# Kernel optimization log

Measured on AMD Instinct MI355X. Metric: run time of the kernel, lower is better.

Reference implementation:

```python
import jax, jax.numpy as jnp
import numpy as np

N_NODES = 50000
N_EDGES = 800000
D_IN = 256
D_HID = 256
D_OUT = 16
N_GRAPHS = 128
DROPOUT_P = 0.5


def setup_inputs() -> dict:
    key = jax.random.key(0)
    ks = jax.random.split(key, 8)
    x = jax.random.normal(ks[0], (N_NODES, D_IN), dtype=jnp.float32)
    edge_index = jax.random.randint(ks[1], (2, N_EDGES), 0, N_NODES, dtype=jnp.int64)
    edge_weight = jax.random.uniform(ks[2], (N_EDGES,), dtype=jnp.float32)
    index = jnp.sort(jax.random.randint(ks[3], (N_NODES,), 0, N_GRAPHS, dtype=jnp.int64))
    W1 = jax.random.normal(ks[4], (D_IN, D_HID), dtype=jnp.float32) / np.sqrt(D_IN)
    b1 = jnp.zeros((D_HID,), dtype=jnp.float32)
    fc_W = jax.random.normal(ks[5], (D_HID, D_OUT), dtype=jnp.float32) / np.sqrt(D_HID)
    fc_b = jnp.zeros((D_OUT,), dtype=jnp.float32)
    return {"x": x, "edge_index": edge_index, "edge_weight": edge_weight,
            "index": index, "W1": W1, "b1": b1, "fc_W": fc_W, "fc_b": fc_b}


def gcn_conv(x, edge_index, edge_weight, W, b):
    # PyG GCNConv: add self loops (weight 1), symmetric degree norm, linear-then-propagate.
    n = x.shape[0]
    loops = jnp.arange(n, dtype=edge_index.dtype)
    row = jnp.concatenate([edge_index[0], loops])   # source nodes
    col = jnp.concatenate([edge_index[1], loops])   # target nodes (aggregation)
    ew = jnp.concatenate([edge_weight, jnp.ones((n,), dtype=x.dtype)])
    deg = jax.ops.segment_sum(ew, col, num_segments=n)
    dinv = jnp.where(deg > 0, jax.lax.rsqrt(deg), 0.0)
    norm = dinv[row] * ew * dinv[col]               # [E+N]
    h = x @ W                                       # [N, hid]
    msg = norm[:, None] * h[row]                    # gather + scale
    out = jax.ops.segment_sum(msg, col, num_segments=n)  # scatter-add
    return out + b


def reference(x, edge_index, edge_weight, index, W1, b1, fc_W, fc_b):
    h = gcn_conv(x, edge_index, edge_weight, W1, b1)
    h = jax.nn.relu(h)
    # dropout (training mode, p=0.5) with a fixed key for determinism
    keep = jax.random.bernoulli(jax.random.key(42), 1.0 - DROPOUT_P, h.shape)
    h = jnp.where(keep, h / (1.0 - DROPOUT_P), 0.0)
    # global mean pool over graph ids
    sums = jax.ops.segment_sum(h, index, num_segments=N_GRAPHS)          # [G, hid]
    cnts = jax.ops.segment_sum(jnp.ones((h.shape[0],), h.dtype), index, num_segments=N_GRAPHS)
    pooled = sums / jnp.maximum(cnts, 1.0)[:, None]
    return pooled @ fc_W + fc_b
```

## Files before the change

kernel.cpp:

```cpp
#include <hip/hip_runtime.h>
#include <hip/hip_fp16.h>
#include <stdint.h>

#define N_NODES  50000
#define N_EDGES  800000
#define D        256
#define D_OUT    16
#define N_GRAPHS 128
#define NB_SCAN  196


typedef short bf16x8 __attribute__((ext_vector_type(8)));
typedef float f32x4  __attribute__((ext_vector_type(4)));
typedef float f32x2  __attribute__((ext_vector_type(2)));

__device__ __forceinline__ uint32_t rotl32(uint32_t x, int d) {
    return (x << d) | (x >> (32 - d));
}

__device__ __forceinline__ void threefry2x32(uint32_t k0, uint32_t k1,
                                             uint32_t c0, uint32_t c1,
                                             uint32_t& o0, uint32_t& o1) {
    uint32_t ks2 = k0 ^ k1 ^ 0x1BD11BDAu;
    uint32_t x0 = c0 + k0, x1 = c1 + k1;
    x0 += x1; x1 = rotl32(x1, 13); x1 ^= x0;
    x0 += x1; x1 = rotl32(x1, 15); x1 ^= x0;
    x0 += x1; x1 = rotl32(x1, 26); x1 ^= x0;
    x0 += x1; x1 = rotl32(x1, 6);  x1 ^= x0;
    x0 += k1; x1 += ks2 + 1u;
    x0 += x1; x1 = rotl32(x1, 17); x1 ^= x0;
    x0 += x1; x1 = rotl32(x1, 29); x1 ^= x0;
    x0 += x1; x1 = rotl32(x1, 16); x1 ^= x0;
    x0 += x1; x1 = rotl32(x1, 24); x1 ^= x0;
    x0 += ks2; x1 += k0 + 2u;
    x0 += x1; x1 = rotl32(x1, 13); x1 ^= x0;
    x0 += x1; x1 = rotl32(x1, 15); x1 ^= x0;
    x0 += x1; x1 = rotl32(x1, 26); x1 ^= x0;
    x0 += x1; x1 = rotl32(x1, 6);  x1 ^= x0;
    x0 += k0; x1 += k1 + 3u;
    x0 += x1; x1 = rotl32(x1, 17); x1 ^= x0;
    x0 += x1; x1 = rotl32(x1, 29); x1 ^= x0;
    x0 += x1; x1 = rotl32(x1, 16); x1 ^= x0;
    x0 += x1; x1 = rotl32(x1, 24); x1 ^= x0;
    x0 += k1; x1 += ks2 + 4u;
    x0 += x1; x1 = rotl32(x1, 13); x1 ^= x0;
    x0 += x1; x1 = rotl32(x1, 15); x1 ^= x0;
    x0 += x1; x1 = rotl32(x1, 26); x1 ^= x0;
    x0 += x1; x1 = rotl32(x1, 6);  x1 ^= x0;
    x0 += ks2; x1 += k0 + 5u;
    o0 = x0; o1 = x1;
}

__device__ __forceinline__ bool dropout_keep(uint32_t i) {
    uint32_t o0, o1;
    threefry2x32(0u, 42u, 0u, i, o0, o1);
    return ((o0 ^ o1) & 0x80000000u) == 0u;
}

__device__ __forceinline__ uint32_t bf16_rne(float f) {
    uint32_t u = __float_as_uint(f);
    return (u + 0x7FFFu + ((u >> 16) & 1u)) >> 16;
}

__global__ __launch_bounds__(256) void k_init(const float* __restrict__ W,
                                              ushort* __restrict__ wt,
                                              double* degsum, float* sums,
                                              int2* __restrict__ edge) {
    int t = threadIdx.x;
    if (blockIdx.x < 16) {
        __shared__ float td[64][65];
        int kb = blockIdx.x & 3, nb = blockIdx.x >> 2;
        int nl = t & 63, r4 = t >> 6;
#pragma unroll
        for (int i = 0; i < 16; i++) {
            int kl = r4 + 4 * i;
            td[kl][nl] = W[(size_t)(kb * 64 + kl) * 256 + nb * 64 + nl];
        }
        __syncthreads();
        int kp = t & 31, nl2 = t >> 5;
        uint32_t* wt32 = (uint32_t*)wt;
#pragma unroll
        for (int i = 0; i < 8; i++) {
            int n = nl2 + 8 * i;
            uint32_t p = bf16_rne(td[2 * kp][n]) | (bf16_rne(td[2 * kp + 1][n]) << 16);
            wt32[((size_t)(nb * 64 + n) * 256 + kb * 64 + 2 * kp) >> 1] = p;
        }
    } else {
        int i = (blockIdx.x - 16) * 256 + t;
        if (i < N_NODES) degsum[i] = 0.0;
        if (i < N_GRAPHS * D) sums[i] = 0.0f;
        if (i < 16) edge[N_EDGES + i] = make_int2(0, 0);
    }
}

__global__ __launch_bounds__(256) void k_edeg(const int* __restrict__ ei,
                                              const float* __restrict__ ew,
                                              double* __restrict__ degsum) {
    int e = blockIdx.x * 256 + threadIdx.x;
    int c = ei[N_EDGES + e];
    atomicAdd(&degsum[c], 4294967296.0 + (double)ew[e]);
}

__global__ __launch_bounds__(256) void k_scan1(const double* __restrict__ degsum,
                                               float* __restrict__ dinv,
                                               int* __restrict__ start,
                                               int* __restrict__ partial) {
    __shared__ int sd[256];
    int t = threadIdx.x;
    int i = blockIdx.x * 256 + t;
    int cnt = 0;
    if (i < N_NODES) {
        double val = degsum[i];
        cnt = (int)(val * (1.0 / 4294967296.0));
        float deg = (float)(val - (double)cnt * 4294967296.0) + 1.0f;
        dinv[i] = rsqrtf(deg);
        start[i] = cnt;
    }
    sd[t] = cnt;
    __syncthreads();
    for (int d = 128; d > 0; d >>= 1) {
        if (t < d) sd[t] += sd[t + d];
        __syncthreads();
    }
    if (t == 0) partial[blockIdx.x] = sd[0];
}

__global__ __launch_bounds__(256) void k_scan3(int* __restrict__ start,
                                               const int* __restrict__ partial) {
    __shared__ int sp[256];
    __shared__ int so[256];
    __shared__ int sd[256];
    int t = threadIdx.x;
    int pv = (t < NB_SCAN) ? partial[t] : 0;
    sp[t] = pv; so[t] = pv;
    __syncthreads();
    for (int d = 1; d < 256; d <<= 1) {
        int u = (t >= d) ? sp[t - d] : 0;
        __syncthreads();
        sp[t] += u;
        __syncthreads();
    }
    int base = sp[blockIdx.x] - so[blockIdx.x];

    int i = blockIdx.x * 256 + t;
    int v = (i < N_NODES) ? start[i] : 0;
    sd[t] = v;
    __syncthreads();
    for (int d = 1; d < 256; d <<= 1) {
        int u = (t >= d) ? sd[t - d] : 0;
        __syncthreads();
        sd[t] += u;
        __syncthreads();
    }
    if (i < N_NODES) start[i] = base + sd[t] - v;
}

__global__ __launch_bounds__(256) void k_fill(const int* __restrict__ ei,
                                              const float* __restrict__ ew,
                                              int* __restrict__ start,
                                              int2* __restrict__ edge) {
    int e = blockIdx.x * 256 + threadIdx.x;
    int r = ei[e];
    int c = ei[N_EDGES + e];
    int pos = atomicAdd(&start[c], 1);
    edge[pos] = make_int2(r * 32, __float_as_int(ew[e]));
}

__device__ __forceinline__ int swz(int row, int kByte) {
    return (row << 9) + (kByte ^ ((row & 7) << 4));
}

__global__ __launch_bounds__(256) void k_gemm(const float* __restrict__ x,
                                              const ushort* __restrict__ wt,
                                              const float* __restrict__ dinv,
                                              uint8_t* __restrict__ hb) {
    __shared__ __align__(16) char smem[73728];
    __shared__ float sdinv[64];
    int tid = threadIdx.x;
    int Mbase = blockIdx.x * 64;

    if (tid < 64) {
        int node = Mbase + tid; if (node >= N_NODES) node = N_NODES - 1;
        sdinv[tid] = dinv[node];
    }
    const float4* xv = (const float4*)x;
#pragma unroll
    for (int i = 0; i < 16; i++) {
        int f = tid + i * 256;
        int r = f >> 6;
        int c4 = f & 63;
        int node = Mbase + r; if (node >= N_NODES) node = N_NODES - 1;
        float4 v = xv[(size_t)node * 64 + c4];
        uint32_t p0 = bf16_rne(v.x) | (bf16_rne(v.y) << 16);
        uint32_t p1 = bf16_rne(v.z) | (bf16_rne(v.w) << 16);
        *(uint2*)(smem + swz(r, c4 * 8)) = make_uint2(p0, p1);
    }

    int l = tid & 63;
    int w = tid >> 6;
    int wr = w >> 1, wc = w & 1;
    int lr = l & 15;
    int kg = l >> 4;
    int drow = (l >> 4) * 4;
    int dcol = l & 15;
    const uint4* wt4 = (const uint4*)wt;
    ushort* c_lds = (ushort*)(smem + 65536);

    for (int nb = 0; nb < 4; nb++) {
#pragma unroll
        for (int i = 0; i < 8; i++) {
            int f = tid + i * 256;
            int r = f >> 5;
            int c = f & 31;
            uint4 v = wt4[(size_t)(nb * 64 + r) * 32 + c];
            *(uint4*)(smem + 32768 + swz(r, c * 16)) = v;
        }
        __syncthreads();

        f32x4 acc00 = {0.f, 0.f, 0.f, 0.f};
        f32x4 acc01 = acc00, acc10 = acc00, acc11 = acc00;
#pragma unroll
        for (int ks = 0; ks < 8; ks++) {
            int kB = ks * 64 + kg * 16;
            bf16x8 a0 = *(const bf16x8*)(smem + swz(wr * 32 + lr, kB));
            bf16x8 a1 = *(const bf16x8*)(smem + swz(wr * 32 + 16 + lr, kB));
            bf16x8 b0 = *(const bf16x8*)(smem + 32768 + swz(wc * 32 + lr, kB));
            bf16x8 b1 = *(const bf16x8*)(smem + 32768 + swz(wc * 32 + 16 + lr, kB));
            acc00 = __builtin_amdgcn_mfma_f32_16x16x32_bf16(a0, b0, acc00, 0, 0, 0);
            acc01 = __builtin_amdgcn_mfma_f32_16x16x32_bf16(a0, b1, acc01, 0, 0, 0);
            acc10 = __builtin_amdgcn_mfma_f32_16x16x32_bf16(a1, b0, acc10, 0, 0, 0);
            acc11 = __builtin_amdgcn_mfma_f32_16x16x32_bf16(a1, b1, acc11, 0, 0, 0);
        }
#pragma unroll
        for (int r = 0; r < 4; r++) {
            int lr0 = wr * 32 + drow + r;
            float s0 = sdinv[lr0], s1 = sdinv[lr0 + 16];
            int cc = wc * 32 + dcol;
            __half h00 = __float2half(acc00[r] * s0);
            __half h01 = __float2half(acc01[r] * s0);
            __half h10 = __float2half(acc10[r] * s1);
            __half h11 = __float2half(acc11[r] * s1);
            c_lds[lr0 * 64 + cc]             = *(ushort*)&h00;
            c_lds[lr0 * 64 + cc + 16]        = *(ushort*)&h01;
            c_lds[(lr0 + 16) * 64 + cc]      = *(ushort*)&h10;
            c_lds[(lr0 + 16) * 64 + cc + 16] = *(ushort*)&h11;
        }
        __syncthreads();
#pragma unroll
        for (int i = 0; i < 2; i++) {
            int idx = tid + i * 256;
            int r = idx >> 3;
            int c8 = idx & 7;
            uint4 v = ((const uint4*)c_lds)[idx];
            __half2* hp = (__half2*)&v;
            float f0 = __low2float(hp[0]), f1 = __high2float(hp[0]);
            float f2 = __low2float(hp[1]), f3 = __high2float(hp[1]);
            float f4 = __low2float(hp[2]), f5 = __high2float(hp[2]);
            float f6 = __low2float(hp[3]), f7 = __high2float(hp[3]);
            uint32_t w0 = __builtin_amdgcn_cvt_pk_fp8_f32(f0, f1, 0, false);
            w0 = __builtin_amdgcn_cvt_pk_fp8_f32(f2, f3, w0, true);
            uint32_t w1 = __builtin_amdgcn_cvt_pk_fp8_f32(f4, f5, 0, false);
            w1 = __builtin_amdgcn_cvt_pk_fp8_f32(f6, f7, w1, true);
            int node = Mbase + r;
            if (node < N_NODES)
                *(uint2*)(hb + (size_t)node * 256 + nb * 64 + c8 * 8) =
                    make_uint2(w0, w1);
        }
    }
}

__device__ __forceinline__ void fma8f(float* a, uint2 u, float w) {
    f32x2 p0 = __builtin_amdgcn_cvt_pk_f32_fp8(u.x, false);
    f32x2 p1 = __builtin_amdgcn_cvt_pk_f32_fp8(u.x, true);
    f32x2 p2 = __builtin_amdgcn_cvt_pk_f32_fp8(u.y, false);
    f32x2 p3 = __builtin_amdgcn_cvt_pk_f32_fp8(u.y, true);
    a[0] = fmaf(w, p0.x, a[0]); a[1] = fmaf(w, p0.y, a[1]);
    a[2] = fmaf(w, p1.x, a[2]); a[3] = fmaf(w, p1.y, a[3]);
    a[4] = fmaf(w, p2.x, a[4]); a[5] = fmaf(w, p2.y, a[5]);
    a[6] = fmaf(w, p3.x, a[6]); a[7] = fmaf(w, p3.y, a[7]);
}

__global__ __launch_bounds__(256) void k_agg(const int* __restrict__ start,
                                             const int2* __restrict__ edge,
                                             const uint8_t* __restrict__ hb,
                                             const float* __restrict__ dinv,
                                             const float* __restrict__ b1,
                                             const int* __restrict__ gidx,
                                             float* __restrict__ sums) {
    __shared__ float ls[4][256];
    int wid = threadIdx.x >> 6;
    int l = threadIdx.x & 63;
    int half = l >> 5;
    int cl = l & 31;
    int n = blockIdx.x * 4 + wid;
    const uint2* h8 = (const uint2*)hb;
    int e = start[n];
    int s = (n == 0) ? 0 : start[n - 1];
    int last = e - 1;

    uint2 un = h8[(size_t)n * 32 + cl];
    float4 bv = ((const float4*)b1)[2 * cl + half];
    float dn = dinv[n];
    int gfirst = gidx[blockIdx.x * 4];
    int glast  = gidx[blockIdx.x * 4 + 3];

    int off = 4 * half;
    int col = 8 * cl + off;

    int j = s;
    int2 E0, E1, E2, E3;
    if (j < e) {
        int i0 = j + half;
        E0 = edge[i0];
        E1 = edge[i0 + 2];
        E2 = edge[i0 + 4];
        E3 = edge[i0 + 6];
    }

    uint32_t base = (uint32_t)n * D + (uint32_t)col;
    float m0 = dropout_keep(base + 0u) ? 2.f : 0.f;
    float m1 = dropout_keep(base + 1u) ? 2.f : 0.f;
    float m2 = dropout_keep(base + 2u) ? 2.f : 0.f;
    float m3 = dropout_keep(base + 3u) ? 2.f : 0.f;

    float A0[8] = {0,0,0,0,0,0,0,0}, A1[8] = {0,0,0,0,0,0,0,0};

    for (; j + 8 <= e; j += 8) {
        uint2 u0 = h8[(size_t)(uint32_t)(E0.x + cl)];
        uint2 u1 = h8[(size_t)(uint32_t)(E1.x + cl)];
        uint2 u2 = h8[(size_t)(uint32_t)(E2.x + cl)];
        uint2 u3 = h8[(size_t)(uint32_t)(E3.x + cl)];
        float w0 = __int_as_float(E0.y);
        float w1 = __int_as_float(E1.y);
        float w2 = __int_as_float(E2.y);
        float w3 = __int_as_float(E3.y);
        int i0n = j + 8 + half;
        E0 = edge[i0n];
        E1 = edge[i0n + 2];
        E2 = edge[i0n + 4];
        E3 = edge[i0n + 6];
        fma8f(A0, u0, w0); fma8f(A1, u1, w1);
        fma8f(A0, u2, w2); fma8f(A1, u3, w3);
    }
    if (j < e) {
        uint2 u0 = h8[(size_t)(uint32_t)(E0.x + cl)];
        uint2 u1 = h8[(size_t)(uint32_t)(E1.x + cl)];
        uint2 u2 = h8[(size_t)(uint32_t)(E2.x + cl)];
        uint2 u3 = h8[(size_t)(uint32_t)(E3.x + cl)];
        int x0 = j + half, x1 = x0 + 2, x2 = x0 + 4, x3 = x0 + 6;
        float w0 = x0 <= last ? __int_as_float(E0.y) : 0.f;
        float w1 = x1 <= last ? __int_as_float(E1.y) : 0.f;
        float w2 = x2 <= last ? __int_as_float(E2.y) : 0.f;
        float w3 = x3 <= last ? __int_as_float(E3.y) : 0.f;
        fma8f(A0, u0, w0); fma8f(A1, u1, w1);
        fma8f(A0, u2, w2); fma8f(A1, u3, w3);
    }

    float full[8];
#pragma unroll
    for (int k = 0; k < 8; k++)
        full[k] = A0[k] + A1[k];
#pragma unroll
    for (int k = 0; k < 8; k++)
        full[k] += __shfl_xor(full[k], 32, 64);

    uint32_t word = half ? un.y : un.x;
    f32x2 q0 = __builtin_amdgcn_cvt_pk_f32_fp8(word, false);
    f32x2 q1 = __builtin_amdgcn_cvt_pk_f32_fp8(word, true);
    float v0 = fmaxf(dn * (full[off + 0] + q0.x) + bv.x, 0.f) * m0;
    float v1 = fmaxf(dn * (full[off + 1] + q0.y) + bv.y, 0.f) * m1;
    float v2 = fmaxf(dn * (full[off + 2] + q1.x) + bv.z, 0.f) * m2;
    float v3 = fmaxf(dn * (full[off + 3] + q1.y) + bv.w, 0.f) * m3;

    if (gfirst == glast) {
        *(float4*)&ls[wid][col] = make_float4(v0, v1, v2, v3);
        __syncthreads();
        int t = threadIdx.x;
        float sv = (ls[0][t] + ls[1][t]) + (ls[2][t] + ls[3][t]);
        atomicAdd(&sums[(size_t)gfirst * D + t], sv);
    } else {
        int g = gidx[n];
        float* sg = &sums[(size_t)g * D + col];
        atomicAdd(sg + 0, v0);
        atomicAdd(sg + 1, v1);
        atomicAdd(sg + 2, v2);
        atomicAdd(sg + 3, v3);
    }
}

__global__ __launch_bounds__(256) void k_out(const float* __restrict__ sums,
                                             const int* __restrict__ gidx,
                                             const float* __restrict__ fcW,
                                             const float* __restrict__ fcb,
                                             float* __restrict__ out) {
    __shared__ int sh[2];
    __shared__ float p[D];
    int g = blockIdx.x, t = threadIdx.x;
    if (t == 0) {
        int lo = 0, hi = N_NODES;
        while (lo < hi) { int m = (lo + hi) >> 1; if (gidx[m] < g) lo = m + 1; else hi = m; }
        sh[0] = lo;
        int lo2 = lo; hi = N_NODES;
        while (lo2 < hi) { int m = (lo2 + hi) >> 1; if (gidx[m] < g + 1) lo2 = m + 1; else hi = m; }
        sh[1] = lo2;
    }
    __syncthreads();
    float c = fmaxf((float)(sh[1] - sh[0]), 1.0f);
    p[t] = sums[(size_t)g * D + t] / c;
    __syncthreads();
    if (t < D_OUT) {
        float acc = fcb[t];
        for (int k = 0; k < D; k++)
            acc = fmaf(p[k], fcW[k * D_OUT + t], acc);
        out[g * D_OUT + t] = acc;
    }
}

extern "C" void kernel_launch(void* const* d_in, const int* in_sizes, int n_in,
                              void* d_out, int out_size, void* d_ws, size_t ws_size,
                              hipStream_t stream) {
    const float* x   = (const float*)d_in[0];
    const int*   ei  = (const int*)d_in[1];
    const float* ew  = (const float*)d_in[2];
    const int*   gix = (const int*)d_in[3];
    const float* W1  = (const float*)d_in[4];
    const float* b1  = (const float*)d_in[5];
    const float* fcW = (const float*)d_in[6];
    const float* fcb = (const float*)d_in[7];
    float* out = (float*)d_out;

    float*   ws     = (float*)d_ws;
    float*   dinv   = ws;
    uint8_t* hb     = (uint8_t*)(ws + 65536);
    int2*    edge   = (int2*)(ws + 65536 + 3200000);
    int*     start  = (int*)(edge + N_EDGES + 16);
    int*     partial    = start + 65536;
    ushort*  wt     = (ushort*)(partial + 512);
    float*   sums   = (float*)(wt + 65536);
    double*  degsum = (double*)(sums + 32768);

    k_init<<<NB_SCAN + 16, 256, 0, stream>>>(W1, wt, degsum, sums, edge);
    k_edeg<<<N_EDGES / 256, 256, 0, stream>>>(ei, ew, degsum);
    k_scan1<<<NB_SCAN, 256, 0, stream>>>(degsum, dinv, start, partial);
    k_scan3<<<NB_SCAN, 256, 0, stream>>>(start, partial);
    k_fill<<<N_EDGES / 256, 256, 0, stream>>>(ei, ew, start, edge);
    k_gemm<<<(N_NODES + 63) / 64, 256, 0, stream>>>(x, wt, dinv, hb);
    k_agg<<<N_NODES / 4, 256, 0, stream>>>(start, edge, hb, dinv, b1, gix, sums);
    k_out<<<N_GRAPHS, 256, 0, stream>>>(sums, gix, fcW, fcb, out);
}
```

Baseline: 190.1 us.

## Fuse degree-count into weight prep and CSR fill into GEMM launch

```diff
diff --git a/kernel.cpp b/kernel.cpp
--- a/kernel.cpp
+++ b/kernel.cpp
@@ -8,6 +8,8 @@
 #define D_OUT    16
 #define N_GRAPHS 128
 #define NB_SCAN  196
+#define GEMM_NB  782
+#define FILL_NB  3125
 
 
 typedef short bf16x8 __attribute__((ext_vector_type(8)));
@@ -62,10 +64,11 @@
     return (u + 0x7FFFu + ((u >> 16) & 1u)) >> 16;
 }
 
-__global__ __launch_bounds__(256) void k_init(const float* __restrict__ W,
+__global__ __launch_bounds__(256) void k_prep(const float* __restrict__ W,
                                               ushort* __restrict__ wt,
-                                              double* degsum, float* sums,
-                                              int2* __restrict__ edge) {
+                                              const int* __restrict__ ei,
+                                              const float* __restrict__ ew,
+                                              double* __restrict__ degsum) {
     int t = threadIdx.x;
     if (blockIdx.x < 16) {
         __shared__ float td[64][65];
@@ -86,19 +89,10 @@
             wt32[((size_t)(nb * 64 + n) * 256 + kb * 64 + 2 * kp) >> 1] = p;
         }
     } else {
-        int i = (blockIdx.x - 16) * 256 + t;
-        if (i < N_NODES) degsum[i] = 0.0;
-        if (i < N_GRAPHS * D) sums[i] = 0.0f;
-        if (i < 16) edge[N_EDGES + i] = make_int2(0, 0);
-    }
-}
-
-__global__ __launch_bounds__(256) void k_edeg(const int* __restrict__ ei,
-                                              const float* __restrict__ ew,
-                                              double* __restrict__ degsum) {
-    int e = blockIdx.x * 256 + threadIdx.x;
-    int c = ei[N_EDGES + e];
-    atomicAdd(&degsum[c], 4294967296.0 + (double)ew[e]);
+        int e = (blockIdx.x - 16) * 256 + t;
+        int c = ei[N_EDGES + e];
+        atomicAdd(&degsum[c], 4294967296.0 + (double)ew[e]);
+    }
 }
 
 __global__ __launch_bounds__(256) void k_scan1(const double* __restrict__ degsum,
@@ -155,30 +149,32 @@
     if (i < N_NODES) start[i] = base + sd[t] - v;
 }
 
-__global__ __launch_bounds__(256) void k_fill(const int* __restrict__ ei,
+__device__ __forceinline__ int swz(int row, int kByte) {
+    return (row << 9) + (kByte ^ ((row & 7) << 4));
+}
+
+__global__ __launch_bounds__(256) void k_main(const float* __restrict__ x,
+                                              const ushort* __restrict__ wt,
+                                              const float* __restrict__ dinv,
+                                              uint8_t* __restrict__ hb,
+                                              const int* __restrict__ ei,
                                               const float* __restrict__ ew,
                                               int* __restrict__ start,
                                               int2* __restrict__ edge) {
-    int e = blockIdx.x * 256 + threadIdx.x;
-    int r = ei[e];
-    int c = ei[N_EDGES + e];
-    int pos = atomicAdd(&start[c], 1);
-    edge[pos] = make_int2(r * 32, __float_as_int(ew[e]));
-}
-
-__device__ __forceinline__ int swz(int row, int kByte) {
-    return (row << 9) + (kByte ^ ((row & 7) << 4));
-}
-
-__global__ __launch_bounds__(256) void k_gemm(const float* __restrict__ x,
-                                              const ushort* __restrict__ wt,
-                                              const float* __restrict__ dinv,
-                                              uint8_t* __restrict__ hb) {
     __shared__ __align__(16) char smem[73728];
     __shared__ float sdinv[64];
     int tid = threadIdx.x;
+
+    if (blockIdx.x >= GEMM_NB) {
+        int e = (blockIdx.x - GEMM_NB) * 256 + tid;
+        int r = ei[e];
+        int c = ei[N_EDGES + e];
+        int pos = atomicAdd(&start[c], 1);
+        edge[pos] = make_int2(r * 32, __float_as_int(ew[e]));
+        return;
+    }
+
     int Mbase = blockIdx.x * 64;
-
     if (tid < 64) {
         int node = Mbase + tid; if (node >= N_NODES) node = N_NODES - 1;
         sdinv[tid] = dinv[node];
@@ -439,12 +435,14 @@
     float*   sums   = (float*)(wt + 65536);
     double*  degsum = (double*)(sums + 32768);
 
-    k_init<<<NB_SCAN + 16, 256, 0, stream>>>(W1, wt, degsum, sums, edge);
-    k_edeg<<<N_EDGES / 256, 256, 0, stream>>>(ei, ew, degsum);
+    hipMemsetAsync(degsum, 0, N_NODES * sizeof(double), stream);
+    hipMemsetAsync(sums, 0, N_GRAPHS * D * sizeof(float), stream);
+    hipMemsetAsync(edge + N_EDGES, 0, 16 * sizeof(int2), stream);
+
+    k_prep<<<16 + FILL_NB, 256, 0, stream>>>(W1, wt, ei, ew, degsum);
     k_scan1<<<NB_SCAN, 256, 0, stream>>>(degsum, dinv, start, partial);
     k_scan3<<<NB_SCAN, 256, 0, stream>>>(start, partial);
-    k_fill<<<N_EDGES / 256, 256, 0, stream>>>(ei, ew, start, edge);
-    k_gemm<<<(N_NODES + 63) / 64, 256, 0, stream>>>(x, wt, dinv, hb);
+    k_main<<<GEMM_NB + FILL_NB, 256, 0, stream>>>(x, wt, dinv, hb, ei, ew, start, edge);
     k_agg<<<N_NODES / 4, 256, 0, stream>>>(start, edge, hb, dinv, b1, gix, sums);
     k_out<<<N_GRAPHS, 256, 0, stream>>>(sums, gix, fcW, fcb, out);
 }
```

After: 189.6 us. No clear change (-0.3%).
